# Performance work log

Hardware: AMD Instinct MI355X
Metric: run time of the kernel (lower is better)

## Reference

```python
import jax, jax.numpy as jnp
import numpy as np

U = 100000          # unique pillars
N = 2 * U           # voxels (2 per pillar -> unq_cnt==2, mask all True)
NUM_BINS = 32       # z bins
C_IN = 5
C_HID = 32          # out_channels // 2 in conv1d MLP
C_OUT = 64
R = 4               # channel-attention reduction
K = 7               # bin-attention conv kernel


def setup_inputs() -> dict:
    key = jax.random.key(0)
    ks = jax.random.split(key, 12)
    voxel_features = jax.random.normal(ks[0], (N, C_IN), jnp.float32)
    # each pillar p owns voxels 2p, 2p+1 placed in two distinct bins -> no scatter collision
    bins = (jnp.arange(N, dtype=jnp.int32) % NUM_BINS)
    voxel_coords = jnp.zeros((N, 4), jnp.int32).at[:, 1].set(bins)
    unq_coords = jnp.arange(U, dtype=jnp.int32)
    unq_inv = jnp.arange(N, dtype=jnp.int32) // 2
    unq_cnt = jnp.full((U,), 2, jnp.int32)
    s = 0.3
    return {
        'voxel_features': voxel_features,
        'voxel_coords': voxel_coords,
        'unq_coords': unq_coords,
        'unq_inv': unq_inv,
        'unq_cnt': unq_cnt,
        # up_dimension MLP (Linear(5,32) -> relu -> Linear(32,64))
        'W1': jax.random.normal(ks[1], (C_IN, C_HID), jnp.float32) * s,
        'b1': jnp.zeros((C_HID,), jnp.float32),
        'W2': jax.random.normal(ks[2], (C_HID, C_OUT), jnp.float32) * s,
        'b2': jnp.zeros((C_OUT,), jnp.float32),
        # ZBAM channel-attention shared MLP
        'Wc1': jax.random.normal(ks[3], (C_OUT, C_OUT // R), jnp.float32) * s,
        'bc1': jnp.zeros((C_OUT // R,), jnp.float32),
        'Wc2': jax.random.normal(ks[4], (C_OUT // R, C_OUT), jnp.float32) * s,
        'bc2': jnp.zeros((C_OUT,), jnp.float32),
        # ZBAM bin (spatial) attention: conv1d over bins, 2->1 channels, kernel 7
        'Wsp': jax.random.normal(ks[5], (1, 2, K), jnp.float32) * s,
        'bsp': jnp.zeros((1,), jnp.float32),
    }


def _cbam_forward(voxel_features, W1, b1, W2, b2, Wc1, bc1, Wc2, bc2, Wsp, bsp,
                  voxel_coords, unq_coords, unq_inv, unq_cnt):
    n_pillars = unq_coords.shape[0]
    # --- binning: scatter voxels into (pillar, z-bin) slots ---
    src = jnp.zeros((n_pillars, NUM_BINS, voxel_features.shape[1]), voxel_features.dtype)
    src = src.at[unq_inv, voxel_coords[:, 1]].set(voxel_features)
    occupied_mask = unq_cnt >= 2  # all True by construction -> src[mask] == src
    # --- up_dimension MLP: (U, bins, 5) -> (U, bins, 64) ---
    x = jax.nn.relu(src @ W1 + b1) @ W2 + b2
    x = jnp.transpose(x, (0, 2, 1))  # (U, C, bins)
    # --- ZBAM channel attention ---
    avg_p = x.mean(axis=2)
    max_p = x.max(axis=2)
    mlp = lambda v: jax.nn.relu(v @ Wc1 + bc1) @ Wc2 + bc2
    att_c = jax.nn.sigmoid(mlp(avg_p) + mlp(max_p))  # (U, C)
    x = x * att_c[:, :, None]
    # --- ZBAM bin attention (conv over z-bins) ---
    s = jnp.stack([x.mean(axis=1), x.max(axis=1)], axis=1)  # (U, 2, bins)
    att_s = jax.lax.conv_general_dilated(
        s, Wsp, window_strides=(1,), padding=[(K // 2, K // 2)],
        dimension_numbers=('NCH', 'OIH', 'NCH')) + bsp  # (U, 1, bins)
    x = x * jax.nn.sigmoid(att_s)
    # --- max-pool over bins ---
    return x.max(axis=2), occupied_mask


def reference(voxel_features, voxel_coords, unq_coords, unq_inv, unq_cnt,
              W1, b1, W2, b2, Wc1, bc1, Wc2, bc2, Wsp, bsp):
    return _cbam_forward(voxel_features, W1, b1, W2, b2, Wc1, bc1, Wc2, bc2,
                         Wsp, bsp, voxel_coords, unq_coords, unq_inv, unq_cnt)
```

## Files before the change

kernel.cpp:

```cpp
#include <hip/hip_runtime.h>
#include <math.h>


#define CO 64

__device__ __forceinline__ float sgm(float x) {
  return 1.0f / (1.0f + __expf(-x));
}
template <int PAT>
__device__ __forceinline__ float qadd(float s) {
  int t = __builtin_amdgcn_update_dpp(0, __builtin_bit_cast(int, s),
                                      PAT, 0xf, 0xf, true);
  return s + __builtin_bit_cast(float, t);
}
template <int PAT>
__device__ __forceinline__ float qmaxd(float m) {
  int t = __builtin_amdgcn_update_dpp(__builtin_bit_cast(int, m),
                                      __builtin_bit_cast(int, m),
                                      PAT, 0xf, 0xf, false);
  return fmaxf(m, __builtin_bit_cast(float, t));
}
template <int PAT>
__device__ __forceinline__ float qmind(float m) {
  int t = __builtin_amdgcn_update_dpp(__builtin_bit_cast(int, m),
                                      __builtin_bit_cast(int, m),
                                      PAT, 0xf, 0xf, false);
  return fminf(m, __builtin_bit_cast(float, t));
}
__device__ __forceinline__ float qsum4(float s) { return qadd<0x4E>(qadd<0xB1>(s)); }
__device__ __forceinline__ float qmax4(float m) { return qmaxd<0x4E>(qmaxd<0xB1>(m)); }
__device__ __forceinline__ float qmin4(float m) { return qmind<0x4E>(qmind<0xB1>(m)); }
__device__ __forceinline__ void drain_lds() {
  __builtin_amdgcn_wave_barrier();
  __builtin_amdgcn_s_waitcnt(0xC07F);
  __builtin_amdgcn_wave_barrier();
}

__global__ __launch_bounds__(256) void pack_kernel(
    const float* __restrict__ vf, const int* __restrict__ vcoord,
    const int* __restrict__ unq_inv, float* __restrict__ pvox, int n) {
  int i = blockIdx.x * blockDim.x + threadIdx.x;
  if (i >= n) return;
  int p = unq_inv[i];
  int slot = (i > 0 && unq_inv[i - 1] == p) ? 1 : 0;
  float* dst = pvox + 8 * (size_t)(2 * p + slot);
#pragma unroll
  for (int k = 0; k < 5; ++k) dst[k] = vf[5 * i + k];
  ((int*)dst)[5] = vcoord[4 * i + 1];
}

__global__ __launch_bounds__(256) void cbam_kernel(
    const float* __restrict__ pvox, const int* __restrict__ unq_cnt,
    const float* __restrict__ W1, const float* __restrict__ b1,
    const float* __restrict__ W2, const float* __restrict__ b2,
    const float* __restrict__ Wc1, const float* __restrict__ bc1,
    const float* __restrict__ Wc2, const float* __restrict__ bc2,
    const float* __restrict__ Wsp, const float* __restrict__ bsp,
    float* __restrict__ out, int U, int ngroups, int totalWaves) {
  __shared__ __align__(16) float w2b[2176];
  __shared__ __align__(16) float wc1b[1024];
  __shared__ __align__(16) float wc2b[1024];
  __shared__ __align__(16) float c0b[64], b2b[64], bc2b[64], bc1b[16];
  __shared__ __align__(16) float wsmx[64];
  __shared__ __align__(16) float wtab[16];
  __shared__ __align__(16) float hbuf[4][1152];

  const int tid = threadIdx.x;

  for (int i = tid; i < 2048; i += 256) w2b[(i >> 6) * 68 + (i & 63)] = W2[i];
  for (int i = tid; i < 1024; i += 256) {
    int ch = i >> 4, j = i & 15, qq = ch >> 4, k = ch & 15;
    wc1b[(4 * k + qq) * 16 + j] = Wc1[i];
    wc2b[(4 * k + qq) * 16 + j] = Wc2[j * 64 + ch];
  }
  if (tid < 64) { b2b[tid] = b2[tid]; bc2b[tid] = bc2[tid]; }
  if (tid < 16) bc1b[tid] = bc1[tid];
  if (tid < 32) {
    float sm = 0.0f, sx = 0.0f;
    for (int k = 0; k < 7; ++k)
      if ((unsigned)(tid + k - 3) < 32u) { sm += Wsp[k]; sx += Wsp[7 + k]; }
    wsmx[2 * tid] = sm; wsmx[2 * tid + 1] = sx;
  }
  if (tid < 8) {
    float a = 0.0f, b = 0.0f;
    if (tid < 7) { a = Wsp[tid]; b = Wsp[7 + tid]; }
    wtab[2 * tid] = a; wtab[2 * tid + 1] = b;
  }
  __syncthreads();
  if (tid < 64) {
    float c = b2b[tid];
    for (int j = 0; j < 32; ++j) c += fmaxf(b1[j], 0.0f) * w2b[j * 68 + tid];
    c0b[tid] = c;
  }
  __syncthreads();

  const int wv = tid >> 6, lane = tid & 63;
  const int wave0 = blockIdx.x * 4 + wv;
  float* const hb = hbuf[wv];

  const int j32 = lane & 31, vh = lane >> 5;
  float w1r[5];
#pragma unroll
  for (int i = 0; i < 5; ++i) w1r[i] = W1[i * 32 + j32];
  const float b1r = b1[j32];

  const int q = lane & 3, pp = lane >> 2;

  for (int grp = wave0; grp < ngroups; grp += totalWaves) {
    const int P0 = grp * 16;

    {
      const float4* pv4 = (const float4*)pvox;
      const int vmax = 2 * U - 1;
#pragma unroll
      for (int v = 0; v < 16; ++v) {
        int vg = 2 * P0 + 16 * vh + v;
        vg = vg < vmax ? vg : vmax;
        float4 g1 = pv4[2 * vg];
        float4 g2 = pv4[2 * vg + 1];
        float h = b1r + g1.x * w1r[0] + g1.y * w1r[1] + g1.z * w1r[2] +
                  g1.w * w1r[3] + g2.x * w1r[4];
        const int row = (v & 1) * 16 + 8 * vh + (v >> 1);
        hb[row * 36 + j32] = fmaxf(h, 0.0f);
      }
    }
    drain_lds();

    const int pg = P0 + pp;
    const int pc = pg < U ? pg : (U - 1);
    const int cnt = unq_cnt[pc];
    const bool has2 = (cnt >= 2);
    const int* pvi = (const int*)pvox;
    const int b0 = pvi[(size_t)(2 * pc) * 8 + 5] & 31;
    const int b1raw = pvi[(size_t)(2 * pc + 1) * 8 + 5];
    const int b1e = has2 ? (b1raw & 31) : 64;

    float y0[16], y1[16];
    const float4* b2b4 = (const float4*)b2b;
#pragma unroll
    for (int kb = 0; kb < 4; ++kb) {
      float4 w = b2b4[q * 4 + kb];
      y0[4 * kb] = w.x; y0[4 * kb + 1] = w.y; y0[4 * kb + 2] = w.z; y0[4 * kb + 3] = w.w;
      y1[4 * kb] = w.x; y1[4 * kb + 1] = w.y; y1[4 * kb + 2] = w.z; y1[4 * kb + 3] = w.w;
    }
    const float4* hb4 = (const float4*)hb;
    const float4* w2b4 = (const float4*)w2b;
    float4 h0c = hb4[pp * 9];
    float4 h1c = hb4[(16 + pp) * 9];
#pragma unroll
    for (int jb = 0; jb < 8; ++jb) {
      float4 h0n, h1n;
      if (jb < 7) {
        h0n = hb4[pp * 9 + jb + 1];
        h1n = hb4[(16 + pp) * 9 + jb + 1];
      }
      float h0a[4] = {h0c.x, h0c.y, h0c.z, h0c.w};
      float h1a[4] = {h1c.x, h1c.y, h1c.z, h1c.w};
#pragma unroll
      for (int jj = 0; jj < 4; ++jj) {
        const int j = 4 * jb + jj;
#pragma unroll
        for (int kb = 0; kb < 4; ++kb) {
          float4 w = w2b4[17 * j + 4 * q + kb];
          y0[4 * kb]     += h0a[jj] * w.x; y0[4 * kb + 1] += h0a[jj] * w.y;
          y0[4 * kb + 2] += h0a[jj] * w.z; y0[4 * kb + 3] += h0a[jj] * w.w;
          y1[4 * kb]     += h1a[jj] * w.x; y1[4 * kb + 1] += h1a[jj] * w.y;
          y1[4 * kb + 2] += h1a[jj] * w.z; y1[4 * kb + 3] += h1a[jj] * w.w;
        }
      }
      h0c = h0n; h1c = h1n;
    }
#pragma unroll
    for (int k = 0; k < 16; ++k) y1[k] = has2 ? y1[k] : y0[k];

    float ha[16] = {0}, hm[16] = {0};
    const float kf = has2 ? 30.0f : 31.0f;
    const float inv32 = 1.0f / 32.0f;
    const float4* c04 = (const float4*)c0b;
    const float4* wc14 = (const float4*)wc1b;
#pragma unroll
    for (int kb = 0; kb < 4; ++kb) {
      float4 cq = c04[q * 4 + kb];
      float c0a[4] = {cq.x, cq.y, cq.z, cq.w};
#pragma unroll
      for (int i = 0; i < 4; ++i) {
        const int k = 4 * kb + i;
        const float c0v = c0a[i];
        const float sumy = y0[k] + (has2 ? y1[k] : 0.0f);
        const float avg = fmaf(c0v, kf, sumy) * inv32;
        const float mxv = fmaxf(fmaxf(y0[k], y1[k]), c0v);
#pragma unroll
        for (int jb = 0; jb < 4; ++jb) {
          float4 w = wc14[(4 * k + q) * 4 + jb];
          ha[4 * jb]     += avg * w.x; ha[4 * jb + 1] += avg * w.y;
          ha[4 * jb + 2] += avg * w.z; ha[4 * jb + 3] += avg * w.w;
          hm[4 * jb]     += mxv * w.x; hm[4 * jb + 1] += mxv * w.y;
          hm[4 * jb + 2] += mxv * w.z; hm[4 * jb + 3] += mxv * w.w;
        }
      }
    }
    float g[16];
    const float4* bc14 = (const float4*)bc1b;
#pragma unroll
    for (int jb = 0; jb < 4; ++jb) {
      float4 bb = bc14[jb];
      float bba[4] = {bb.x, bb.y, bb.z, bb.w};
#pragma unroll
      for (int i = 0; i < 4; ++i) {
        const int j = 4 * jb + i;
        const float sa = qsum4(ha[j]) + bba[i];
        const float sm = qsum4(hm[j]) + bba[i];
        g[j] = fmaxf(sa, 0.0f) + fmaxf(sm, 0.0f);
      }
    }

    float attc[16];
    float sc = 0.0f, mc = -3.0e38f;
    float sy0 = 0.0f, my0 = -3.0e38f, sy1 = 0.0f, my1 = -3.0e38f;
    const float4* wc24 = (const float4*)wc2b;
    const float4* bc24 = (const float4*)bc2b;
#pragma unroll
    for (int kb = 0; kb < 4; ++kb) {
      float4 cq = c04[q * 4 + kb];
      float4 bq = bc24[q * 4 + kb];
      float c0a[4] = {cq.x, cq.y, cq.z, cq.w};
      float b2a[4] = {bq.x, bq.y, bq.z, bq.w};
#pragma unroll
      for (int i = 0; i < 4; ++i) {
        const int k = 4 * kb + i;
        float pre = 2.0f * b2a[i];
#pragma unroll
        for (int jb = 0; jb < 4; ++jb) {
          float4 w = wc24[(4 * k + q) * 4 + jb];
          pre += g[4 * jb] * w.x + g[4 * jb + 1] * w.y +
                 g[4 * jb + 2] * w.z + g[4 * jb + 3] * w.w;
        }
        const float a = sgm(pre);
        attc[k] = a;
        const float pc0 = a * c0a[i], py0 = a * y0[k], py1 = a * y1[k];
        sc += pc0;  mc = fmaxf(mc, pc0);
        sy0 += py0; my0 = fmaxf(my0, py0);
        sy1 += py1; my1 = fmaxf(my1, py1);
      }
    }
    sc = qsum4(sc);   mc = qmax4(mc);
    sy0 = qsum4(sy0); my0 = qmax4(my0);
    sy1 = qsum4(sy1); my1 = qmax4(my1);

    const float inv64 = 1.0f / 64.0f;
    const float Mn = sc * inv64, Mx = mc;
    const float dm0 = (sy0 - sc) * inv64, dx0 = my0 - mc;
    const float dm1 = (sy1 - sc) * inv64, dx1 = my1 - mc;
    const float bspr = bsp[0];
    const float2* ws2 = (const float2*)wsmx;
    const float2* wt2 = (const float2*)wtab;
    float maxE = -3.0e38f, minE = 3.0e38f, sv0 = -3.0e38f, sv1 = -3.0e38f;
#pragma unroll
    for (int k = 0; k < 8; ++k) {
      const int b = 8 * q + k;
      float2 ws = ws2[b];
      float acc = bspr + Mn * ws.x + Mx * ws.y;
      int k0 = b0 - b + 3;  k0 = ((unsigned)k0 <= 6u) ? k0 : 7;
      int k1 = b1e - b + 3; k1 = ((unsigned)k1 <= 6u) ? k1 : 7;
      float2 w0 = wt2[k0];
      float2 w1v = wt2[k1];
      acc += dm0 * w0.x + dx0 * w0.y + dm1 * w1v.x + dx1 * w1v.y;
      const bool o0 = (b == b0), o1 = (b == b1e);
      const bool oc = o0 || o1;
      maxE = fmaxf(maxE, oc ? -3.0e38f : acc);
      minE = fminf(minE, oc ?  3.0e38f : acc);
      sv0 = o0 ? acc : sv0;
      sv1 = o1 ? acc : sv1;
    }
    maxE = qmax4(maxE); minE = qmin4(minE);
    sv0 = qmax4(sv0);   sv1 = qmax4(sv1);
    const float sig0 = sgm(sv0);
    const float sig1 = has2 ? sgm(sv1) : sig0;
    const float sE = sgm(maxE), sI = sgm(minE);

    if (pg < U) {
      float4* ov = (float4*)(out + (size_t)pg * CO + 16 * q);
#pragma unroll
      for (int kb = 0; kb < 4; ++kb) {
        float4 cq = c04[q * 4 + kb];
        float c0a[4] = {cq.x, cq.y, cq.z, cq.w};
        float rr[4];
#pragma unroll
        for (int i = 0; i < 4; ++i) {
          const int k = 4 * kb + i;
          const float c0v = c0a[i];
          const float sel = (c0v >= 0.0f) ? sE : sI;
          const float m = fmaxf(fmaxf(y0[k] * sig0, y1[k] * sig1), c0v * sel);
          rr[i] = attc[k] * m;
        }
        float4 r; r.x = rr[0]; r.y = rr[1]; r.z = rr[2]; r.w = rr[3];
        ov[kb] = r;
      }
      if (q == 0) out[(size_t)U * CO + pg] = has2 ? 1.0f : 0.0f;
    }
    drain_lds();
  }
}

extern "C" void kernel_launch(void* const* d_in, const int* in_sizes, int n_in,
                              void* d_out, int out_size, void* d_ws, size_t ws_size,
                              hipStream_t stream) {
  const float* vf      = (const float*)d_in[0];
  const int*   vcoord  = (const int*)d_in[1];
  const int*   unq_inv = (const int*)d_in[3];
  const int*   unq_cnt = (const int*)d_in[4];
  const float* W1  = (const float*)d_in[5];
  const float* b1  = (const float*)d_in[6];
  const float* W2  = (const float*)d_in[7];
  const float* b2  = (const float*)d_in[8];
  const float* Wc1 = (const float*)d_in[9];
  const float* bc1 = (const float*)d_in[10];
  const float* Wc2 = (const float*)d_in[11];
  const float* bc2 = (const float*)d_in[12];
  const float* Wsp = (const float*)d_in[13];
  const float* bsp = (const float*)d_in[14];

  const int N = in_sizes[3];
  const int U = in_sizes[4];

  float* pvox = (float*)d_ws;

  pack_kernel<<<(N + 255) / 256, 256, 0, stream>>>(vf, vcoord, unq_inv, pvox, N);

  const int ngroups = (U + 15) / 16;
  int blocks = 1024;
  const int maxBlocks = (ngroups + 3) / 4;
  if (blocks > maxBlocks) blocks = maxBlocks;
  const int totalWaves = blocks * 4;
  cbam_kernel<<<blocks, 256, 0, stream>>>(
      pvox, unq_cnt, W1, b1, W2, b2, Wc1, bc1, Wc2, bc2, Wsp, bsp,
      (float*)d_out, U, ngroups, totalWaves);
}
```

Baseline: 147.6 us.

## Prefetch next group's voxel records into LDS while computing current group

Each wave now loads its next group's 16-pillar voxel block (64 float4s, one per lane) into a register at the start of an iteration and writes it into a per-wave LDS buffer at the end. The current group's first-layer MLP and the bin-index reads come from LDS instead of scattered global loads. This is meant to hide global memory latency behind the compute of the current group. The W2 LDS padding (stride 68) is also removed in favour of a dense stride-64 layout, which may bring back bank conflicts on the float4 weight reads.

After: 146.2 us. Within noise of the previous version (-1.0%).

```diff
diff --git a/kernel.cpp b/kernel.cpp
--- a/kernel.cpp
+++ b/kernel.cpp
@@ -57,17 +57,18 @@
     const float* __restrict__ Wc2, const float* __restrict__ bc2,
     const float* __restrict__ Wsp, const float* __restrict__ bsp,
     float* __restrict__ out, int U, int ngroups, int totalWaves) {
-  __shared__ __align__(16) float w2b[2176];
+  __shared__ __align__(16) float w2b[2048];
   __shared__ __align__(16) float wc1b[1024];
   __shared__ __align__(16) float wc2b[1024];
   __shared__ __align__(16) float c0b[64], b2b[64], bc2b[64], bc1b[16];
   __shared__ __align__(16) float wsmx[64];
   __shared__ __align__(16) float wtab[16];
   __shared__ __align__(16) float hbuf[4][1152];
+  __shared__ __align__(16) float vbuf[4][256];
 
   const int tid = threadIdx.x;
 
-  for (int i = tid; i < 2048; i += 256) w2b[(i >> 6) * 68 + (i & 63)] = W2[i];
+  for (int i = tid; i < 2048; i += 256) w2b[i] = W2[i];
   for (int i = tid; i < 1024; i += 256) {
     int ch = i >> 4, j = i & 15, qq = ch >> 4, k = ch & 15;
     wc1b[(4 * k + qq) * 16 + j] = Wc1[i];
@@ -89,14 +90,15 @@
   __syncthreads();
   if (tid < 64) {
     float c = b2b[tid];
-    for (int j = 0; j < 32; ++j) c += fmaxf(b1[j], 0.0f) * w2b[j * 68 + tid];
+    for (int j = 0; j < 32; ++j) c += fmaxf(b1[j], 0.0f) * w2b[j * 64 + tid];
     c0b[tid] = c;
   }
   __syncthreads();
 
   const int wv = tid >> 6, lane = tid & 63;
-  const int wave0 = blockIdx.x * 4 + wv;
   float* const hb = hbuf[wv];
+  float* const vb = vbuf[wv];
+  float4* const vb4 = (float4*)vb;
 
   const int j32 = lane & 31, vh = lane >> 5;
   float w1r[5];
@@ -105,19 +107,37 @@
   const float b1r = b1[j32];
 
   const int q = lane & 3, pp = lane >> 2;
-
-  for (int grp = wave0; grp < ngroups; grp += totalWaves) {
+  const float4* pv4 = (const float4*)pvox;
+  const int f4max = 4 * U - 1;
+
+  {
+    int idx = 64 * (blockIdx.x * 4 + wv) + lane;
+    idx = idx < f4max ? idx : f4max;
+    vb4[lane] = pv4[idx];
+  }
+  drain_lds();
+
+  for (int grp = blockIdx.x * 4 + wv; grp < ngroups; grp += totalWaves) {
     const int P0 = grp * 16;
 
+    int nidx = 64 * (grp + totalWaves) + lane;
+    nidx = nidx < f4max ? nidx : f4max;
+    const float4 pfn = pv4[nidx];
+
+    const int pg = P0 + pp;
+    const int pc = pg < U ? pg : (U - 1);
+    const int cnt = unq_cnt[pc];
+    const int* vbi = (const int*)vb;
+    const int b0 = vbi[(2 * pp) * 8 + 5] & 31;
+    const int b1raw = vbi[(2 * pp + 1) * 8 + 5];
+
     {
-      const float4* pv4 = (const float4*)pvox;
-      const int vmax = 2 * U - 1;
+      const float4* vb4c = (const float4*)vb;
 #pragma unroll
       for (int v = 0; v < 16; ++v) {
-        int vg = 2 * P0 + 16 * vh + v;
-        vg = vg < vmax ? vg : vmax;
-        float4 g1 = pv4[2 * vg];
-        float4 g2 = pv4[2 * vg + 1];
+        const int rec = 16 * vh + v;
+        float4 g1 = vb4c[2 * rec];
+        float4 g2 = vb4c[2 * rec + 1];
         float h = b1r + g1.x * w1r[0] + g1.y * w1r[1] + g1.z * w1r[2] +
                   g1.w * w1r[3] + g2.x * w1r[4];
         const int row = (v & 1) * 16 + 8 * vh + (v >> 1);
@@ -126,13 +146,7 @@
     }
     drain_lds();
 
-    const int pg = P0 + pp;
-    const int pc = pg < U ? pg : (U - 1);
-    const int cnt = unq_cnt[pc];
     const bool has2 = (cnt >= 2);
-    const int* pvi = (const int*)pvox;
-    const int b0 = pvi[(size_t)(2 * pc) * 8 + 5] & 31;
-    const int b1raw = pvi[(size_t)(2 * pc + 1) * 8 + 5];
     const int b1e = has2 ? (b1raw & 31) : 64;
 
     float y0[16], y1[16];
@@ -161,7 +175,7 @@
         const int j = 4 * jb + jj;
 #pragma unroll
         for (int kb = 0; kb < 4; ++kb) {
-          float4 w = w2b4[17 * j + 4 * q + kb];
+          float4 w = w2b4[16 * j + 4 * q + kb];
           y0[4 * kb]     += h0a[jj] * w.x; y0[4 * kb + 1] += h0a[jj] * w.y;
           y0[4 * kb + 2] += h0a[jj] * w.z; y0[4 * kb + 3] += h0a[jj] * w.w;
           y1[4 * kb]     += h1a[jj] * w.x; y1[4 * kb + 1] += h1a[jj] * w.y;
@@ -298,6 +312,8 @@
       }
       if (q == 0) out[(size_t)U * CO + pg] = has2 ? 1.0f : 0.0f;
     }
+
+    vb4[lane] = pfn;
     drain_lds();
   }
 }
```
